# Kernel optimization log

Hardware: AMD Instinct MI355X
Metric: run time of the kernel (lower is better)

## Reference

```python
import jax, jax.numpy as jnp
import numpy as np

MIN_RATIO, MAX_RATIO = 0.7, 1.3
MIN_BIAS, MAX_BIAS = -4.0, 4.0
SOFTMAX_SCALE = 3.0


def setup_inputs() -> dict:
    key = jax.random.key(0)
    k1, k2, k3 = jax.random.split(key, 3)
    B, L_org, N = 32, 2048, 21
    org_tensor = jax.random.normal(k1, (B, L_org, N), dtype=jnp.float32)
    # small perturbations so the clamps are active but not saturated
    ratio_minus_one = 0.1 * jax.random.normal(k2, (N,), dtype=jnp.float32)
    bias = 0.5 * jax.random.normal(k3, (N,), dtype=jnp.float32)
    return {"org_tensor": org_tensor, "ratio_minus_one": ratio_minus_one,
            "bias": bias, "to_length": 2048}


def reference(org_tensor, ratio_minus_one, bias, to_length):
    # input_transformation with is_mark=False
    B, L_org, N = org_tensor.shape
    L_to = to_length
    dt = org_tensor.dtype
    # relu-based clamping in the original == clip
    ratio = jnp.clip(ratio_minus_one + 1.0, MIN_RATIO, MAX_RATIO)  # [N]
    b = jnp.clip(bias, MIN_BIAS, MAX_BIAS)                         # [N]
    org_pos = jnp.arange(-L_org, 0, dtype=dt)                      # [L_org]
    # transformed positions are batch-independent: [L_org, N, 1]
    tpos = org_pos[:, None, None] * ratio[None, :, None] + b[None, :, None]
    tgt = jnp.arange(-L_to, 0, dtype=dt)                           # [L_to]
    deltas = (tpos - tgt[None, None, :]) ** 2                      # [L_org, N, L_to]
    weights = jax.nn.softmax(-deltas * SOFTMAX_SCALE, axis=0)      # softmax over L_org
    # einsum 'bont,bon->btn' with batch-independent weights
    out = jnp.einsum('ont,bon->btn', weights, org_tensor)          # [B, L_to, N]
    return out
```

## Files before the change

kernel.cpp:

```cpp
#include <hip/hip_runtime.h>
#include <hip/hip_bf16.h>


constexpr int LORG  = 2048;
constexpr int LTO   = 2048;
constexpr int NCH   = 21;
constexpr int BATCH = 32;
constexpr int W     = 8;
constexpr int NW    = 2 * W + 1;
constexpr int TT    = 64;
constexpr int BH    = 16;
constexpr int XSTR  = 113;
constexpr int NBLK  = NCH * (LTO / TT) * (BATCH / BH);

constexpr float MIN_RATIO = 0.7f, MAX_RATIO = 1.3f;
constexpr float MIN_BIAS  = -4.0f, MAX_BIAS = 4.0f;
constexpr float NEG3LOG2E = -3.0f * 1.4426950408889634f;

__device__ __forceinline__ int compute_o0(float tg, float bb, float ir) {
    const float ocf = (float)LORG + (tg - bb) * ir;
    int o0 = (int)floorf(ocf + 0.5f) - W;
    return max(0, min(LORG - NW, o0));
}

__global__ __launch_bounds__(256) void li_fused(
    const float* __restrict__ x,
    const float* __restrict__ rmo,
    const float* __restrict__ bias,
    float* __restrict__ out)
{
    const int h  = blockIdx.x;
    const int wk = (h & 7) * (NBLK / 8) + (h >> 3);
    const int bh = wk & 1;
    const int tn = wk >> 1;
    const int tt = tn / NCH;
    const int n  = tn - tt * NCH;
    const int t0 = tt * TT;

    const int tid = threadIdx.x;
    const int tl  = tid & 63;
    const int wv  = tid >> 6;
    const int b0  = bh * BH;

    __shared__ float xs[BH][XSTR];

    const float r  = fminf(fmaxf(rmo[n] + 1.0f, MIN_RATIO), MAX_RATIO);
    const float bb = fminf(fmaxf(bias[n], MIN_BIAS), MAX_BIAS);
    const float ir = 1.0f / r;

    const int lo  = compute_o0((float)(t0 - LTO), bb, ir);
    const int hi  = compute_o0((float)(t0 + TT - 1 - LTO), bb, ir);
    const int len = hi + NW - lo;

    const float tg = (float)(t0 + tl - LTO);
    const int   o0 = compute_o0(tg, bb, ir);
    const int base = o0 - lo;
    float d = (float)(o0 - LORG) * r + bb - tg;
    float js = floorf(-d * ir + 0.5f);
    js = fminf(fmaxf(js, 0.0f), 16.0f);
    const float dstar = d + js * r;
    const float m = NEG3LOG2E * dstar * dstar;
    float w[NW];
    float s = 0.0f;
    #pragma unroll
    for (int j = 0; j < NW; ++j) {
        const float e = NEG3LOG2E * d * d - m;
        w[j] = exp2f(e);
        s += w[j];
        d += r;
    }
    const float inv = 1.0f / s;

    for (int bl = wv; bl < BH; bl += 4) {
        const float* col = x + ((size_t)((b0 + bl) * LORG + lo)) * NCH + n;
        for (int i = tl; i < len; i += 64)
            xs[bl][i] = col[(size_t)i * NCH];
    }
    __syncthreads();

    for (int bl = wv; bl < BH; bl += 4) {
        float acc = 0.0f;
        #pragma unroll
        for (int j = 0; j < NW; ++j)
            acc = fmaf(w[j], xs[bl][base + j], acc);
        out[((size_t)(b0 + bl) * LTO + t0 + tl) * NCH + n] = acc * inv;
    }
}

extern "C" void kernel_launch(void* const* d_in, const int* in_sizes, int n_in,
                              void* d_out, int out_size, void* d_ws, size_t ws_size,
                              hipStream_t stream) {
    const float* x    = (const float*)d_in[0];
    const float* rmo  = (const float*)d_in[1];
    const float* bias = (const float*)d_in[2];
    float* out = (float*)d_out;

    li_fused<<<NBLK, 256, 0, stream>>>(x, rmo, bias, out);
}
```

Baseline: 17.67 us.

## Pre-transpose input to channel-major workspace before interpolation gather

Adds a transpose kernel that rewrites the [B, L, N] input into an [N, B, L] workspace buffer. The interpolation kernel can then read each channel column contiguously instead of with a stride of 21 floats. The aim is to replace uncoalesced strided global loads with coalesced ones. The cost is an extra kernel launch plus a full read and write of the 5.5 MB input, with the fused kernel kept as a fallback when the workspace is too small.

```diff
diff --git a/kernel.cpp b/kernel.cpp
--- a/kernel.cpp
+++ b/kernel.cpp
@@ -10,8 +10,7 @@
 constexpr int NW    = 2 * W + 1;
 constexpr int TT    = 64;
 constexpr int BH    = 16;
-constexpr int XSTR  = 113;
-constexpr int NBLK  = NCH * (LTO / TT) * (BATCH / BH);
+constexpr int XSTR  = 108;
 
 constexpr float MIN_RATIO = 0.7f, MAX_RATIO = 1.3f;
 constexpr float MIN_BIAS  = -4.0f, MAX_BIAS = 4.0f;
@@ -23,24 +22,34 @@
     return max(0, min(LORG - NW, o0));
 }
 
-__global__ __launch_bounds__(256) void li_fused(
-    const float* __restrict__ x,
+__global__ __launch_bounds__(256) void li_transpose(
+    const float* __restrict__ x, float* __restrict__ xt)
+{
+    const int b  = blockIdx.y;
+    const int o0 = blockIdx.x * 64;
+    __shared__ float tile[64 * NCH];
+    const float* src = x + ((size_t)b * LORG + o0) * NCH;
+    for (int i = threadIdx.x; i < 64 * NCH; i += 256) tile[i] = src[i];
+    __syncthreads();
+    for (int j = threadIdx.x; j < 64 * NCH; j += 256) {
+        const int n = j >> 6, k = j & 63;
+        xt[((size_t)(n * BATCH + b)) * LORG + o0 + k] = tile[k * NCH + n];
+    }
+}
+
+__global__ __launch_bounds__(256) void li_interp(
+    const float* __restrict__ xt,
     const float* __restrict__ rmo,
     const float* __restrict__ bias,
     float* __restrict__ out)
 {
-    const int h  = blockIdx.x;
-    const int wk = (h & 7) * (NBLK / 8) + (h >> 3);
-    const int bh = wk & 1;
-    const int tn = wk >> 1;
-    const int tt = tn / NCH;
-    const int n  = tn - tt * NCH;
-    const int t0 = tt * TT;
+    const int t0 = blockIdx.x * TT;
+    const int b0 = blockIdx.y * BH;
+    const int n  = blockIdx.z;
 
     const int tid = threadIdx.x;
     const int tl  = tid & 63;
-    const int wv  = tid >> 6;
-    const int b0  = bh * BH;
+    const int bg  = tid >> 6;
 
     __shared__ float xs[BH][XSTR];
 
@@ -48,6 +57,69 @@
     const float bb = fminf(fmaxf(bias[n], MIN_BIAS), MAX_BIAS);
     const float ir = 1.0f / r;
 
+    const int lo  = compute_o0((float)(t0 - LTO), bb, ir);
+    const int hi  = compute_o0((float)(t0 + TT - 1 - LTO), bb, ir);
+    const int len = hi + NW - lo;
+
+    const float tg = (float)(t0 + tl - LTO);
+    const int   o0 = compute_o0(tg, bb, ir);
+    const int base = o0 - lo;
+    float d = (float)(o0 - LORG) * r + bb - tg;
+    float js = floorf(-d * ir + 0.5f);
+    js = fminf(fmaxf(js, 0.0f), 16.0f);
+    const float dstar = d + js * r;
+    const float m = NEG3LOG2E * dstar * dstar;
+    float w[NW];
+    float s = 0.0f;
+    #pragma unroll
+    for (int j = 0; j < NW; ++j) {
+        const float e = NEG3LOG2E * d * d - m;
+        w[j] = exp2f(e);
+        s += w[j];
+        d += r;
+    }
+    const float inv = 1.0f / s;
+
+    const float* colbase = xt + ((size_t)n * BATCH + b0) * LORG + lo;
+    for (int idx = tid; idx < BH * 128; idx += 256) {
+        const int bl = idx >> 7, i = idx & 127;
+        if (i < len) xs[bl][i] = colbase[(size_t)bl * LORG + i];
+    }
+    __syncthreads();
+
+    for (int bl = bg; bl < BH; bl += 4) {
+        float acc = 0.0f;
+        #pragma unroll
+        for (int j = 0; j < NW; ++j)
+            acc = fmaf(w[j], xs[bl][base + j], acc);
+        out[((size_t)(b0 + bl) * LTO + t0 + tl) * NCH + n] = acc * inv;
+    }
+}
+
+__global__ __launch_bounds__(256) void li_fused(
+    const float* __restrict__ x,
+    const float* __restrict__ rmo,
+    const float* __restrict__ bias,
+    float* __restrict__ out)
+{
+    const int h   = blockIdx.x;
+    const int NB  = NCH * (LTO / TT) * (BATCH / BH);
+    const int wk  = (h & 7) * (NB / 8) + (h >> 3);
+    const int bh  = wk & 1;
+    const int tn  = wk >> 1;
+    const int tt  = tn / NCH;
+    const int n   = tn - tt * NCH;
+    const int t0  = tt * TT;
+    const int tid = threadIdx.x;
+    const int tl  = tid & 63;
+    const int wv  = tid >> 6;
+    const int b0  = bh * BH;
+
+    __shared__ float xs[BH][113];
+
+    const float r  = fminf(fmaxf(rmo[n] + 1.0f, MIN_RATIO), MAX_RATIO);
+    const float bb = fminf(fmaxf(bias[n], MIN_BIAS), MAX_BIAS);
+    const float ir = 1.0f / r;
     const int lo  = compute_o0((float)(t0 - LTO), bb, ir);
     const int hi  = compute_o0((float)(t0 + TT - 1 - LTO), bb, ir);
     const int len = hi + NW - lo;
@@ -95,5 +167,13 @@
     const float* bias = (const float*)d_in[2];
     float* out = (float*)d_out;
 
-    li_fused<<<NBLK, 256, 0, stream>>>(x, rmo, bias, out);
+    const size_t xt_bytes = (size_t)NCH * BATCH * LORG * sizeof(float);
+    if (ws_size >= xt_bytes) {
+        float* xt = (float*)d_ws;
+        li_transpose<<<dim3(LORG / 64, BATCH), 256, 0, stream>>>(x, xt);
+        li_interp<<<dim3(LTO / TT, BATCH / BH, NCH), 256, 0, stream>>>(xt, rmo, bias, out);
+    } else {
+        const int NB = NCH * (LTO / TT) * (BATCH / BH);
+        li_fused<<<NB, 256, 0, stream>>>(x, rmo, bias, out);
+    }
 }
```

Measured after the change: 20.89 us. 1.18x slower.

## Double-buffer per-wave shared staging and drop block-wide barrier

Applied to the files above, without the earlier changes.

Each wave now stages its own batch rows in a private double-buffered shared slice. It prefetches the next row's window into registers while computing the current row, which removes the block-level __syncthreads. Loads are clamped to len-1 so each lane issues exactly two loads per row, with no loop. This relies on the window length never exceeding 128 and on wave-level lockstep for ordering in LDS. There is no explicit intra-wave barrier, which is a subtle correctness assumption.

```diff
diff --git a/kernel.cpp b/kernel.cpp
--- a/kernel.cpp
+++ b/kernel.cpp
@@ -10,7 +10,6 @@
 constexpr int NW    = 2 * W + 1;
 constexpr int TT    = 64;
 constexpr int BH    = 16;
-constexpr int XSTR  = 113;
 constexpr int NBLK  = NCH * (LTO / TT) * (BATCH / BH);
 
 constexpr float MIN_RATIO = 0.7f, MAX_RATIO = 1.3f;
@@ -42,7 +41,7 @@
     const int wv  = tid >> 6;
     const int b0  = bh * BH;
 
-    __shared__ float xs[BH][XSTR];
+    __shared__ float xs[4][2][128];
 
     const float r  = fminf(fmaxf(rmo[n] + 1.0f, MIN_RATIO), MAX_RATIO);
     const float bb = fminf(fmaxf(bias[n], MIN_BIAS), MAX_BIAS);
@@ -71,19 +70,37 @@
     }
     const float inv = 1.0f / s;
 
-    for (int bl = wv; bl < BH; bl += 4) {
-        const float* col = x + ((size_t)((b0 + bl) * LORG + lo)) * NCH + n;
-        for (int i = tl; i < len; i += 64)
-            xs[bl][i] = col[(size_t)i * NCH];
+    const int i0 = min(tl,      len - 1);
+    const int i1 = min(tl + 64, len - 1);
+
+    {
+        const float* col = x + ((size_t)((b0 + wv) * LORG + lo)) * NCH + n;
+        const float v0 = col[(size_t)i0 * NCH];
+        const float v1 = col[(size_t)i1 * NCH];
+        xs[wv][0][tl]      = v0;
+        xs[wv][0][tl + 64] = v1;
     }
-    __syncthreads();
 
-    for (int bl = wv; bl < BH; bl += 4) {
+    #pragma unroll
+    for (int k = 0; k < 4; ++k) {
+        const int bl = wv + 4 * k;
+        float v0 = 0.0f, v1 = 0.0f;
+        if (k < 3) {
+            const float* col = x + ((size_t)((b0 + bl + 4) * LORG + lo)) * NCH + n;
+            v0 = col[(size_t)i0 * NCH];
+            v1 = col[(size_t)i1 * NCH];
+        }
+
         float acc = 0.0f;
         #pragma unroll
         for (int j = 0; j < NW; ++j)
-            acc = fmaf(w[j], xs[bl][base + j], acc);
+            acc = fmaf(w[j], xs[wv][k & 1][base + j], acc);
         out[((size_t)(b0 + bl) * LTO + t0 + tl) * NCH + n] = acc * inv;
+
+        if (k < 3) {
+            xs[wv][(k + 1) & 1][tl]      = v0;
+            xs[wv][(k + 1) & 1][tl + 64] = v1;
+        }
     }
 }
 
```

New measurement: 16.85 us. 1.05x faster.

## Issue input loads before weight math, use per-wave LDS, drop barrier

Applied to the files above, without the earlier changes.

Halves the batch chunk per block to 8, giving more blocks, with each wave handling two batch rows. The strided global loads of the input column are issued before the Gaussian weight computation so memory latency overlaps the exp2 math. Each wave now writes and reads its own shared-memory slice, so the block-wide __syncthreads is removed. Outputs are written with nontemporal stores. The code assumes the needed input window fits in 128 entries and that wave-local LDS ordering makes the barrier unnecessary.

```diff
diff --git a/kernel.cpp b/kernel.cpp
--- a/kernel.cpp
+++ b/kernel.cpp
@@ -9,8 +9,7 @@
 constexpr int W     = 8;
 constexpr int NW    = 2 * W + 1;
 constexpr int TT    = 64;
-constexpr int BH    = 16;
-constexpr int XSTR  = 113;
+constexpr int BH    = 8;
 constexpr int NBLK  = NCH * (LTO / TT) * (BATCH / BH);
 
 constexpr float MIN_RATIO = 0.7f, MAX_RATIO = 1.3f;
@@ -31,8 +30,8 @@
 {
     const int h  = blockIdx.x;
     const int wk = (h & 7) * (NBLK / 8) + (h >> 3);
-    const int bh = wk & 1;
-    const int tn = wk >> 1;
+    const int bh = wk & 3;
+    const int tn = wk >> 2;
     const int tt = tn / NCH;
     const int n  = tn - tt * NCH;
     const int t0 = tt * TT;
@@ -42,7 +41,7 @@
     const int wv  = tid >> 6;
     const int b0  = bh * BH;
 
-    __shared__ float xs[BH][XSTR];
+    __shared__ float xs[4][2][128];
 
     const float r  = fminf(fmaxf(rmo[n] + 1.0f, MIN_RATIO), MAX_RATIO);
     const float bb = fminf(fmaxf(bias[n], MIN_BIAS), MAX_BIAS);
@@ -51,6 +50,18 @@
     const int lo  = compute_o0((float)(t0 - LTO), bb, ir);
     const int hi  = compute_o0((float)(t0 + TT - 1 - LTO), bb, ir);
     const int len = hi + NW - lo;
+
+    const int i0 = min(tl,      len - 1);
+    const int i1 = min(tl + 64, len - 1);
+
+    const int ba = b0 + wv;
+    const int bc = b0 + wv + 4;
+    const float* colA = x + ((size_t)(ba * LORG + lo)) * NCH + n;
+    const float* colC = x + ((size_t)(bc * LORG + lo)) * NCH + n;
+    const float a0 = colA[(size_t)i0 * NCH];
+    const float a1 = colA[(size_t)i1 * NCH];
+    const float c0 = colC[(size_t)i0 * NCH];
+    const float c1 = colC[(size_t)i1 * NCH];
 
     const float tg = (float)(t0 + tl - LTO);
     const int   o0 = compute_o0(tg, bb, ir);
@@ -71,20 +82,21 @@
     }
     const float inv = 1.0f / s;
 
-    for (int bl = wv; bl < BH; bl += 4) {
-        const float* col = x + ((size_t)((b0 + bl) * LORG + lo)) * NCH + n;
-        for (int i = tl; i < len; i += 64)
-            xs[bl][i] = col[(size_t)i * NCH];
+    xs[wv][0][tl]      = a0;
+    xs[wv][0][tl + 64] = a1;
+    xs[wv][1][tl]      = c0;
+    xs[wv][1][tl + 64] = c1;
+
+    float accA = 0.0f, accC = 0.0f;
+    #pragma unroll
+    for (int j = 0; j < NW; ++j) {
+        accA = fmaf(w[j], xs[wv][0][base + j], accA);
+        accC = fmaf(w[j], xs[wv][1][base + j], accC);
     }
-    __syncthreads();
-
-    for (int bl = wv; bl < BH; bl += 4) {
-        float acc = 0.0f;
-        #pragma unroll
-        for (int j = 0; j < NW; ++j)
-            acc = fmaf(w[j], xs[bl][base + j], acc);
-        out[((size_t)(b0 + bl) * LTO + t0 + tl) * NCH + n] = acc * inv;
-    }
+    __builtin_nontemporal_store(accA * inv,
+        out + ((size_t)ba * LTO + t0 + tl) * NCH + n);
+    __builtin_nontemporal_store(accC * inv,
+        out + ((size_t)bc * LTO + t0 + tl) * NCH + n);
 }
 
 extern "C" void kernel_launch(void* const* d_in, const int* in_sizes, int n_in,
```

Result: slower. 26.88 us (+52.1%).
